# Kernel tuning notes

Hardware: AMD Instinct MI355X
Metric: run time of the kernel (lower is better)

Reference implementation:

```python
import jax, jax.numpy as jnp
import numpy as np
from jax import lax

NT = 100
NUM_LEVELS = 9

_KERNEL = jnp.array([[0.0, 0.25, 0.0],
                     [0.25, 0.0, 0.25],
                     [0.0, 0.25, 0.0]], dtype=jnp.float32).reshape(1, 1, 3, 3)


def _conv(x):
    # 3x3 Jacobi stencil, padding=1 (SAME), NCHW layout
    return lax.conv_general_dilated(x, _KERNEL.astype(x.dtype), (1, 1), 'SAME',
                                    dimension_numbers=('NCHW', 'OIHW', 'NCHW'))


def _avg_pool2(x):
    n, c, h, w = x.shape
    return x.reshape(n, c, h // 2, 2, w // 2, 2).mean(axis=(3, 5))


def _interp(x, th, tw):
    n, c = x.shape[:2]
    # bilinear, align_corners=False (half-pixel centers) == jax.image bilinear
    return jax.image.resize(x, (n, c, th, tw), method='bilinear')


def _jacobi(x, mask, nt):
    def step(x, _):
        x_next = _conv(x)
        return x_next * mask + x * (1 - mask), None
    x, _ = lax.scan(step, x, None, length=nt)
    return x


def setup_inputs() -> dict:
    key = jax.random.key(0)
    ks = jax.random.split(key, 12)
    inp = {'X': jax.random.normal(ks[0], (1, 1, 1024, 1024), dtype=jnp.float32)}
    sizes = [1024, 512, 256, 128, 64, 32, 16, 8, 4, 4]
    for i, s in enumerate(sizes):
        inp[f'Mask{i + 1}'] = jax.random.uniform(ks[i + 1], (1, 1, s, s), dtype=jnp.float32)
    return inp


def reference(X, Mask1, Mask2, Mask3, Mask4, Mask5, Mask6, Mask7, Mask8, Mask9, Mask10):
    masks = [Mask1, Mask2, Mask3, Mask4, Mask5, Mask6, Mask7, Mask8, Mask9, Mask10]
    grids = [X]
    # Restriction sweep: fine -> coarse
    for level in range(1, NUM_LEVELS):
        g = grids[level - 1]
        m = masks[level - 1]
        masked_out = _conv(g * (m > 0).astype(g.dtype))
        unmasked_out = _conv(g * (1 - m))
        residual = masked_out + unmasked_out
        grids.append(_avg_pool2(residual))
    # Coarse solve: Jacobi relaxation on coarsest grid with Mask9
    grids[-1] = _jacobi(grids[-1], Mask9, NT)
    # Prolongation sweep: coarse -> fine
    for level in range(NUM_LEVELS - 2, -1, -1):
        th, tw = grids[level].shape[-2:]
        fine = _interp(grids[level + 1], th, tw) + grids[level]
        m = masks[level]
        fine = _conv(fine * (m > 0).astype(fine.dtype)) + _conv(fine * (1 - m))
        grids[level + 1] = fine  # mirror torch list mutation semantics loosely
    # torch code pops down to grids[0] (original X) and runs fine Jacobi on it
    final_solution = grids[0]
    final_solution = _jacobi(final_solution, Mask1, NT)
    return final_solution
```

## Files before the change

### kernel.cpp

```cpp
#include <hip/hip_runtime.h>


#define W 1024
#define H 1024
#define TILE_W 128
#define TILE_H 64
#define TI 10
#define OS_X 104
#define OS_Y 44
#define HX 12
#define NBX 10
#define NBY 24
#define NLAUNCH 10

typedef unsigned uint2v __attribute__((ext_vector_type(2)));

__device__ __forceinline__ float4 ld4(const float* __restrict__ p, int gr, int gc) {
    if ((unsigned)gr < (unsigned)H && (unsigned)gc < (unsigned)W)
        return *(const float4*)&p[gr * W + gc];
    return make_float4(0.f, 0.f, 0.f, 0.f);
}

__device__ __forceinline__ float4 rowstep(const float4 up, const float4 ce,
                                          const float4 dn, const float lf,
                                          const float rt, const float4 m) {
    float4 s, n;
    s.x = (up.x + dn.x) + (lf   + ce.y);
    s.y = (up.y + dn.y) + (ce.x + ce.z);
    s.z = (up.z + dn.z) + (ce.y + ce.w);
    s.w = (up.w + dn.w) + (ce.z + rt);
    n.x = fmaf(m.x, fmaf(0.25f, s.x, -ce.x), ce.x);
    n.y = fmaf(m.y, fmaf(0.25f, s.y, -ce.y), ce.y);
    n.z = fmaf(m.z, fmaf(0.25f, s.z, -ce.z), ce.z);
    n.w = fmaf(m.w, fmaf(0.25f, s.w, -ce.w), ce.w);
    return n;
}

__device__ __forceinline__ float xchg32(float p) {
    unsigned u = __float_as_uint(p);
    uint2v r = __builtin_amdgcn_permlane32_swap(u, u, false, false);
    return __uint_as_float(r.x ^ r.y ^ u);
}

__device__ __forceinline__ float4 xchg32_4(const float4 p) {
    return make_float4(xchg32(p.x), xchg32(p.y), xchg32(p.z), xchg32(p.w));
}

__device__ __forceinline__ float4 sel4(bool c, const float4 a, const float4 b) {
    return make_float4(c ? a.x : b.x, c ? a.y : b.y,
                       c ? a.z : b.z, c ? a.w : b.w);
}

__shared__ float4 SLs[2][18][34];
__shared__ float4 SRs[2][18][34];
__shared__ float4 STs[2][10][32];
__shared__ float4 SBs[2][10][32];

template <int RB, bool PUB>
__device__ __forceinline__ void one_iter(
    int pr, int pc, int wid, bool lowHalf,
    float4 (&c)[4], const float4 (&m)[4])
{
    const float4 p4 = sel4(lowHalf, c[3], c[0]);
    const float4 q4 = xchg32_4(p4);

    float4 th = q4, bh = q4;
    if (lowHalf) th = SBs[RB][wid][pc];
    else         bh = STs[RB][wid + 2][pc];

    const float4 lh = SRs[RB][pr + 1][pc];
    const float4 rh = SLs[RB][pr + 1][pc + 2];

    const float4 n0 = rowstep(th,   c[0], c[1], lh.x, rh.x, m[0]);
    const float4 n1 = rowstep(c[0], c[1], c[2], lh.y, rh.y, m[1]);
    const float4 n2 = rowstep(c[1], c[2], c[3], lh.z, rh.z, m[2]);
    const float4 n3 = rowstep(c[2], c[3], bh,   lh.w, rh.w, m[3]);
    c[0] = n0; c[1] = n1; c[2] = n2; c[3] = n3;

    if (PUB) {
        constexpr int WB = RB ^ 1;
        SLs[WB][pr + 1][pc + 1] = make_float4(n0.x, n1.x, n2.x, n3.x);
        SRs[WB][pr + 1][pc + 1] = make_float4(n0.w, n1.w, n2.w, n3.w);
        if (lowHalf) STs[WB][wid + 1][pc] = n0;
        else         SBs[WB][wid + 1][pc] = n3;
        __syncthreads();
    }
}

__global__ __launch_bounds__(512, 1) void jacobi_trap(
    const float* __restrict__ xin, const float* __restrict__ mask,
    float* __restrict__ xout)
{
    const int tid = threadIdx.x;
    const int pr  = tid >> 5;
    const int pc  = tid & 31;
    const int wid = tid >> 6;
    const bool lowHalf = (tid & 32) == 0;
    const int gx0 = (int)blockIdx.x * OS_X - HX;
    const int gy0 = (int)blockIdx.y * OS_Y - TI;
    const int gr0 = gy0 + pr * 4;
    const int gc0 = gx0 + pc * 4;

    float4 c[4], m[4];
    #pragma unroll
    for (int i = 0; i < 4; ++i) {
        c[i] = ld4(xin,  gr0 + i, gc0);
        m[i] = ld4(mask, gr0 + i, gc0);
    }

    const float4 z4 = make_float4(0.f, 0.f, 0.f, 0.f);
    if (tid < 72) {
        int b = tid / 36, r2 = tid % 36;
        if (r2 < 18) SRs[b][r2][0] = z4;
        else         SLs[b][r2 - 18][33] = z4;
    } else if (tid >= 128 && tid < 256) {
        int j = tid - 128, b = j >> 6, r3 = j & 63;
        if (r3 < 32) STs[b][9][r3] = z4;
        else         SBs[b][0][r3 - 32] = z4;
    }

    SLs[0][pr + 1][pc + 1] = make_float4(c[0].x, c[1].x, c[2].x, c[3].x);
    SRs[0][pr + 1][pc + 1] = make_float4(c[0].w, c[1].w, c[2].w, c[3].w);
    if (lowHalf) STs[0][wid + 1][pc] = c[0];
    else         SBs[0][wid + 1][pc] = c[3];
    __syncthreads();

    one_iter<0, true >(pr, pc, wid, lowHalf, c, m);
    one_iter<1, true >(pr, pc, wid, lowHalf, c, m);
    one_iter<0, true >(pr, pc, wid, lowHalf, c, m);
    one_iter<1, true >(pr, pc, wid, lowHalf, c, m);
    one_iter<0, true >(pr, pc, wid, lowHalf, c, m);
    one_iter<1, true >(pr, pc, wid, lowHalf, c, m);
    one_iter<0, true >(pr, pc, wid, lowHalf, c, m);
    one_iter<1, true >(pr, pc, wid, lowHalf, c, m);
    one_iter<0, true >(pr, pc, wid, lowHalf, c, m);
    one_iter<1, false>(pr, pc, wid, lowHalf, c, m);

    const int lc = pc * 4;
    if (lc >= HX && lc < HX + OS_X && (unsigned)gc0 < (unsigned)W) {
        #pragma unroll
        for (int i = 0; i < 4; ++i) {
            int lr = pr * 4 + i;
            if (lr < TI || lr >= TILE_H - TI) continue;
            int gr = gy0 + lr;
            if ((unsigned)gr >= (unsigned)H) continue;
            *(float4*)&xout[gr * W + gc0] = c[i];
        }
    }
}

extern "C" void kernel_launch(void* const* d_in, const int* in_sizes, int n_in,
                              void* d_out, int out_size, void* d_ws, size_t ws_size,
                              hipStream_t stream) {
    const float* X = (const float*)d_in[0];
    const float* M = (const float*)d_in[1];
    float* out = (float*)d_out;
    float* ws  = (float*)d_ws;

    dim3 grid(NBX, NBY), block(512);
    const float* src = X;
    for (int l = 0; l < NLAUNCH; ++l) {
        float* dst = (l & 1) ? out : ws;
        jacobi_trap<<<grid, block, 0, stream>>>(src, M, dst);
        src = dst;
    }
}
```

Measured before the change: 101.1 us.

## Replace block-wide barriers with per-wave neighbor flags in Jacobi trapezoid

```diff
diff --git a/kernel.cpp b/kernel.cpp
--- a/kernel.cpp
+++ b/kernel.cpp
@@ -12,6 +12,7 @@
 #define NBX 10
 #define NBY 24
 #define NLAUNCH 10
+#define FBIG 0x3fffffff
 
 typedef unsigned uint2v __attribute__((ext_vector_type(2)));
 
@@ -55,12 +56,18 @@
 __shared__ float4 SRs[2][18][34];
 __shared__ float4 STs[2][10][32];
 __shared__ float4 SBs[2][10][32];
+__shared__ int    wflag[10];
 
 template <int RB, bool PUB>
 __device__ __forceinline__ void one_iter(
-    int pr, int pc, int wid, bool lowHalf,
+    int j, int pr, int pc, int wid, int lane, bool lowHalf,
     float4 (&c)[4], const float4 (&m)[4])
 {
+    while (__hip_atomic_load(&wflag[wid], __ATOMIC_ACQUIRE,
+                             __HIP_MEMORY_SCOPE_WORKGROUP) < j ||
+           __hip_atomic_load(&wflag[wid + 2], __ATOMIC_ACQUIRE,
+                             __HIP_MEMORY_SCOPE_WORKGROUP) < j) {}
+
     const float4 p4 = sel4(lowHalf, c[3], c[0]);
     const float4 q4 = xchg32_4(p4);
 
@@ -83,7 +90,9 @@
         SRs[WB][pr + 1][pc + 1] = make_float4(n0.w, n1.w, n2.w, n3.w);
         if (lowHalf) STs[WB][wid + 1][pc] = n0;
         else         SBs[WB][wid + 1][pc] = n3;
-        __syncthreads();
+        if (lane == 0)
+            __hip_atomic_store(&wflag[wid + 1], j + 1, __ATOMIC_RELEASE,
+                               __HIP_MEMORY_SCOPE_WORKGROUP);
     }
 }
 
@@ -95,6 +104,7 @@
     const int pr  = tid >> 5;
     const int pc  = tid & 31;
     const int wid = tid >> 6;
+    const int lane = tid & 63;
     const bool lowHalf = (tid & 32) == 0;
     const int gx0 = (int)blockIdx.x * OS_X - HX;
     const int gy0 = (int)blockIdx.y * OS_Y - TI;
@@ -117,6 +127,9 @@
         int j = tid - 128, b = j >> 6, r3 = j & 63;
         if (r3 < 32) STs[b][9][r3] = z4;
         else         SBs[b][0][r3 - 32] = z4;
+    } else if (tid >= 256 && tid < 266) {
+        int f = tid - 256;
+        wflag[f] = (f == 0 || f == 9) ? FBIG : 0;
     }
 
     SLs[0][pr + 1][pc + 1] = make_float4(c[0].x, c[1].x, c[2].x, c[3].x);
@@ -125,16 +138,16 @@
     else         SBs[0][wid + 1][pc] = c[3];
     __syncthreads();
 
-    one_iter<0, true >(pr, pc, wid, lowHalf, c, m);
-    one_iter<1, true >(pr, pc, wid, lowHalf, c, m);
-    one_iter<0, true >(pr, pc, wid, lowHalf, c, m);
-    one_iter<1, true >(pr, pc, wid, lowHalf, c, m);
-    one_iter<0, true >(pr, pc, wid, lowHalf, c, m);
-    one_iter<1, true >(pr, pc, wid, lowHalf, c, m);
-    one_iter<0, true >(pr, pc, wid, lowHalf, c, m);
-    one_iter<1, true >(pr, pc, wid, lowHalf, c, m);
-    one_iter<0, true >(pr, pc, wid, lowHalf, c, m);
-    one_iter<1, false>(pr, pc, wid, lowHalf, c, m);
+    one_iter<0, true >(0, pr, pc, wid, lane, lowHalf, c, m);
+    one_iter<1, true >(1, pr, pc, wid, lane, lowHalf, c, m);
+    one_iter<0, true >(2, pr, pc, wid, lane, lowHalf, c, m);
+    one_iter<1, true >(3, pr, pc, wid, lane, lowHalf, c, m);
+    one_iter<0, true >(4, pr, pc, wid, lane, lowHalf, c, m);
+    one_iter<1, true >(5, pr, pc, wid, lane, lowHalf, c, m);
+    one_iter<0, true >(6, pr, pc, wid, lane, lowHalf, c, m);
+    one_iter<1, true >(7, pr, pc, wid, lane, lowHalf, c, m);
+    one_iter<0, true >(8, pr, pc, wid, lane, lowHalf, c, m);
+    one_iter<1, false>(9, pr, pc, wid, lane, lowHalf, c, m);
 
     const int lc = pc * 4;
     if (lc >= HX && lc < HX + OS_X && (unsigned)gc0 < (unsigned)W) {
```

New measurement: 107.8 us. 1.07x slower.
